# Kernel tuning notes

Hardware: AMD Instinct MI355X
Metric: run time of the kernel (lower is better)

## Reference

```python
import jax, jax.numpy as jnp
import numpy as np


def setup_inputs() -> dict:
    key = jax.random.key(0)
    # values near 1 so a 4096-long cumulative product stays numerically sane
    x = 1.0 + 0.001 * jax.random.normal(key, (32, 4096, 512), dtype=jnp.float32)
    return {"x": x, "dim": 1}


def reference(x, dim):
    # cumulative product along `dim` (inclusive scan), same math as torch.cumprod
    return jnp.cumprod(x, axis=dim)
```

## Files before the change

kernel.cpp:

```cpp
#include <hip/hip_runtime.h>


typedef float f4 __attribute__((ext_vector_type(4)));

constexpr int L  = 4096;
constexpr int C  = 512;
constexpr int C4 = C / 4;
constexpr int CG = 8;
constexpr int W  = 64;
constexpr int KE = 8;
constexpr int CL = W * KE;
constexpr int NCHUNK = L / CL;
constexpr int NWAVE = CG * W / 64;
constexpr int WPW = 64 / CG;

__device__ __forceinline__ f4 shflup(f4 v, int lanes) {
    f4 r;
#pragma unroll
    for (int j = 0; j < 4; ++j) r[j] = __shfl_up(v[j], lanes, 64);
    return r;
}

__global__ __launch_bounds__(CG * W, 4)
void cumprod_kernel(const f4* __restrict__ x, f4* __restrict__ out) {
    __shared__ f4 s[2][NWAVE][CG + 1];

    const int tid  = threadIdx.x;
    const int c4   = tid & (CG - 1);
    const int w    = tid >> 3;
    const int lane = tid & 63;
    const int wi   = lane >> 3;
    const int ww   = tid >> 6;
    const int c4g  = blockIdx.x * CG + c4;
    const int b    = blockIdx.y;
    const int base = (b * L) * C4 + c4g;

    f4 carry = {1.f, 1.f, 1.f, 1.f};

    f4 p[KE];
    {
        const int lb = base + (w * KE) * C4;
#pragma unroll
        for (int i = 0; i < KE; ++i)
            p[i] = __builtin_nontemporal_load(&x[lb + i * C4]);
    }

    for (int chunk = 0; chunk < NCHUNK; ++chunk) {
        f4 v[KE];
#pragma unroll
        for (int i = 0; i < KE; ++i) v[i] = p[i];

        if (chunk + 1 < NCHUNK) {
            const int lb = base + ((chunk + 1) * CL + w * KE) * C4;
#pragma unroll
            for (int i = 0; i < KE; ++i)
                p[i] = __builtin_nontemporal_load(&x[lb + i * C4]);
        }

#pragma unroll
        for (int i = 1; i < KE; ++i) v[i] = v[i] * v[i - 1];

        f4 seg = v[KE - 1];
#pragma unroll
        for (int d = 1; d < WPW; d <<= 1) {
            f4 t = shflup(seg, d * CG);
            if (wi >= d) seg = seg * t;
        }

        f4 exw = shflup(seg, CG);

        if (wi == WPW - 1) s[chunk & 1][ww][c4] = seg;

        asm volatile("s_waitcnt lgkmcnt(0)" ::: "memory");
        __builtin_amdgcn_s_barrier();

        f4 wpre = {1.f, 1.f, 1.f, 1.f};
        f4 tot  = {1.f, 1.f, 1.f, 1.f};
#pragma unroll
        for (int j = 0; j < NWAVE; ++j) {
            f4 sj = s[chunk & 1][j][c4];
            if (j < ww) wpre = wpre * sj;
            tot = tot * sj;
        }

        f4 pref = carry * wpre;
        if (wi > 0) pref = pref * exw;

        const int lb = base + (chunk * CL + w * KE) * C4;
#pragma unroll
        for (int i = 0; i < KE; ++i)
            __builtin_nontemporal_store(pref * v[i], &out[lb + i * C4]);

        carry = carry * tot;
    }
}

extern "C" void kernel_launch(void* const* d_in, const int* in_sizes, int n_in,
                              void* d_out, int out_size, void* d_ws, size_t ws_size,
                              hipStream_t stream) {
    const f4* x = (const f4*)d_in[0];
    f4* out = (f4*)d_out;

    const int B = in_sizes[0] / (L * C);

    dim3 grid(C4 / CG, B);
    dim3 block(CG * W);
    cumprod_kernel<<<grid, block, 0, stream>>>(x, out);
}
```

Before: 449.0 us.

## Double column group width and parallelize cross-wave prefix across lanes with xor shuffles

Raises the columns per block from 8 to 16 float4s, so each block has 1024 threads and 16 waves, and each wave holds 4 row-groups instead of 8. The cross-wave combine changes from every lane serially reading all wave totals to each lane reading 4 of the 16 totals and reducing them with xor shuffles. This shortens the per-chunk serial shared-memory loop and widens contiguous memory accesses per row. The cost is larger blocks with fewer resident per CU, heavier register pressure under launch_bounds(1024,4), and half as many blocks in the grid.

```diff
diff --git a/kernel.cpp b/kernel.cpp
--- a/kernel.cpp
+++ b/kernel.cpp
@@ -6,7 +6,7 @@
 constexpr int L  = 4096;
 constexpr int C  = 512;
 constexpr int C4 = C / 4;
-constexpr int CG = 8;
+constexpr int CG = 16;
 constexpr int W  = 64;
 constexpr int KE = 8;
 constexpr int CL = W * KE;
@@ -20,6 +20,12 @@
     for (int j = 0; j < 4; ++j) r[j] = __shfl_up(v[j], lanes, 64);
     return r;
 }
+__device__ __forceinline__ f4 shflxor(f4 v, int mask) {
+    f4 r;
+#pragma unroll
+    for (int j = 0; j < 4; ++j) r[j] = __shfl_xor(v[j], mask, 64);
+    return r;
+}
 
 __global__ __launch_bounds__(CG * W, 4)
 void cumprod_kernel(const f4* __restrict__ x, f4* __restrict__ out) {
@@ -27,9 +33,9 @@
 
     const int tid  = threadIdx.x;
     const int c4   = tid & (CG - 1);
-    const int w    = tid >> 3;
+    const int w    = tid >> 4;
     const int lane = tid & 63;
-    const int wi   = lane >> 3;
+    const int wi   = lane >> 4;
     const int ww   = tid >> 6;
     const int c4g  = blockIdx.x * CG + c4;
     const int b    = blockIdx.y;
@@ -61,12 +67,12 @@
         for (int i = 1; i < KE; ++i) v[i] = v[i] * v[i - 1];
 
         f4 seg = v[KE - 1];
-#pragma unroll
-        for (int d = 1; d < WPW; d <<= 1) {
-            f4 t = shflup(seg, d * CG);
-            if (wi >= d) seg = seg * t;
+        {
+            f4 t = shflup(seg, CG);
+            if (wi >= 1) seg = seg * t;
+            t = shflup(seg, 2 * CG);
+            if (wi >= 2) seg = seg * t;
         }
-
         f4 exw = shflup(seg, CG);
 
         if (wi == WPW - 1) s[chunk & 1][ww][c4] = seg;
@@ -74,16 +80,23 @@
         asm volatile("s_waitcnt lgkmcnt(0)" ::: "memory");
         __builtin_amdgcn_s_barrier();
 
-        f4 wpre = {1.f, 1.f, 1.f, 1.f};
-        f4 tot  = {1.f, 1.f, 1.f, 1.f};
+        f4 pall = {1.f, 1.f, 1.f, 1.f};
+        f4 plt  = {1.f, 1.f, 1.f, 1.f};
 #pragma unroll
-        for (int j = 0; j < NWAVE; ++j) {
+        for (int r = 0; r < 4; ++r) {
+            const int j = wi * 4 + r;
             f4 sj = s[chunk & 1][j][c4];
-            if (j < ww) wpre = wpre * sj;
-            tot = tot * sj;
+            pall = pall * sj;
+            if (j < ww) plt = plt * sj;
+        }
+        {
+            f4 q = shflxor(pall, CG);     pall = pall * q;
+            q = shflxor(pall, 2 * CG);    pall = pall * q;
+            q = shflxor(plt, CG);         plt = plt * q;
+            q = shflxor(plt, 2 * CG);     plt = plt * q;
         }
 
-        f4 pref = carry * wpre;
+        f4 pref = carry * plt;
         if (wi > 0) pref = pref * exw;
 
         const int lb = base + (chunk * CL + w * KE) * C4;
@@ -91,7 +104,7 @@
         for (int i = 0; i < KE; ++i)
             __builtin_nontemporal_store(pref * v[i], &out[lb + i * C4]);
 
-        carry = carry * tot;
+        carry = carry * pall;
     }
 }
 
```

After: 434.3 us. 3.3% less time.
